# Performance work log

Measured on AMD Instinct MI355X. Metric: run time of the kernel, lower is better.

Reference implementation:

```python
import jax, jax.numpy as jnp
import numpy as np

HEADS = 8
C_HEAD = 64  # head dim == in_dim of x
P0, P1 = 2, 3  # adaptive pool output


def setup_inputs() -> dict:
    key = jax.random.key(0)
    ks = jax.random.split(key, 8)
    b, c, h, w = 16, 64, 64, 96
    m, d = 6, 192
    inner = HEADS * C_HEAD  # 512
    return {
        "x": jax.random.normal(ks[0], (b, c, h, w), dtype=jnp.float32),
        "z": jax.random.normal(ks[1], (b, m, d), dtype=jnp.float32),
        "conv_w": jax.random.normal(ks[2], (192, c), dtype=jnp.float32) * 0.02,
        "conv_b": jax.random.normal(ks[3], (192,), dtype=jnp.float32) * 0.02,
        "wq": jax.random.normal(ks[4], (d, inner), dtype=jnp.float32) * 0.02,
        "bq": jax.random.normal(ks[5], (inner,), dtype=jnp.float32) * 0.02,
        "wo": jax.random.normal(ks[6], (inner, d), dtype=jnp.float32) * 0.02,
        "bo": jax.random.normal(ks[7], (d,), dtype=jnp.float32) * 0.02,
    }


def reference(x, z, conv_w, conv_b, wq, bq, wo, bo):
    b, c, h, w = x.shape
    _, m, d = z.shape
    # 1x1 conv (pointwise GEMM over channels) + bias
    xp = jnp.einsum('bchw,oc->bohw', x, conv_w) + conv_b[None, :, None, None]
    # AdaptiveAvgPool2d((2,3)) with exact divisibility -> block mean
    xp = xp.reshape(b, 192, P0, h // P0, P1, w // P1).mean(axis=(3, 5))  # [b,192,2,3]
    # view(b, d, m) then permute(0,2,1) -> [b, m, d]
    z = z + xp.reshape(b, d, m).transpose(0, 2, 1)
    # k = v: view(b, h*w, c), repeat heads along last dim, view(b, heads, h*w, c)
    # (row-major reshape reproduces torch .view semantics exactly)
    kv = jnp.tile(x.reshape(b, h * w, c), (1, 1, HEADS)).reshape(b, HEADS, h * w, C_HEAD)
    # q = Linear(dim, heads*c) then view(b, heads, m, c)
    q = (z @ wq + bq).reshape(b, HEADS, m, C_HEAD)
    scale = C_HEAD ** -0.5
    dots = jnp.einsum('bhmc,bhlc->bhml', q, kv) * scale  # [b,h,m,l]
    attn = jax.nn.softmax(dots, axis=-1)
    out = jnp.einsum('bhml,bhlc->bhmc', attn, kv)
    out = out.transpose(0, 2, 1, 3).reshape(b, m, HEADS * C_HEAD)  # b m (h c)
    return z + out @ wo + bo
```

## Files before the change

### kernel.cpp

```cpp
#include <hip/hip_runtime.h>

#define NB 16
#define NC 64
#define NM 6
#define ND 192
#define NHEADS 8
#define NCH 64
#define NINNER 512
#define PLANE 6144
#define XB (NC*PLANE)
#define NKEY 768
#define NCHUNK 8
#define CK 96
#define KP 68
#define SP 100

__global__ __launch_bounds__(256) void pool_kernel(const float* __restrict__ x,
                                                   float* __restrict__ xmean) {
    int bc = blockIdx.x;
    const float4* p = (const float4*)(x + (size_t)bc * PLANE);
    int tid = threadIdx.x;
    float acc[6] = {0.f,0.f,0.f,0.f,0.f,0.f};
    #pragma unroll
    for (int k = 0; k < 6; ++k) {
        int idx4 = tid + k * 256;
        int hh = idx4 / 24;
        int w4 = idx4 - hh * 24;
        int j = (hh >> 5) * 3 + (w4 >> 3);
        float4 v = p[idx4];
        acc[j] += v.x + v.y + v.z + v.w;
    }
    int lane = tid & 63, wave = tid >> 6;
    #pragma unroll
    for (int j = 0; j < 6; ++j) {
        float v = acc[j];
        for (int off = 32; off > 0; off >>= 1) v += __shfl_down(v, off, 64);
        acc[j] = v;
    }
    __shared__ float part[4][6];
    if (lane == 0) {
        #pragma unroll
        for (int j = 0; j < 6; ++j) part[wave][j] = acc[j];
    }
    __syncthreads();
    if (tid < 6) {
        float s = part[0][tid] + part[1][tid] + part[2][tid] + part[3][tid];
        xmean[bc * 6 + tid] = s * (1.0f / 1024.0f);
    }
}

__global__ __launch_bounds__(256) void zq_kernel(const float* __restrict__ z,
                                                 const float* __restrict__ conv_w,
                                                 const float* __restrict__ conv_b,
                                                 const float* __restrict__ wq,
                                                 const float* __restrict__ bq,
                                                 const float* __restrict__ xmean,
                                                 float* __restrict__ znew,
                                                 float* __restrict__ qr) {
    int blk = blockIdx.x;
    int cgrp = blk & 7, bm = blk >> 3;
    int b = bm / NM, m = bm - b * NM;
    int tid = threadIdx.x;
    __shared__ float xm[NC];
    __shared__ float zn[ND];
    __shared__ float qpart[3][64];
    if (tid < NC) xm[tid] = xmean[(b * NC + tid) * NM + m];
    __syncthreads();
    if (tid < ND) {
        float a = conv_b[tid];
        const float* wr = conv_w + tid * NC;
        #pragma unroll 16
        for (int c = 0; c < NC; ++c) a += wr[c] * xm[c];
        float v = z[bm * ND + tid] + a;
        zn[tid] = v;
        if (cgrp == 0) znew[bm * ND + tid] = v;
    }
    __syncthreads();
    int colL = tid & 63, ks = tid >> 6;
    int col = cgrp * 64 + colL;
    float a = (ks == 0) ? bq[col] : 0.f;
    int d0 = ks * 48;
    #pragma unroll 8
    for (int d = d0; d < d0 + 48; ++d) a += zn[d] * wq[d * NINNER + col];
    if (ks > 0) qpart[ks - 1][colL] = a;
    __syncthreads();
    if (ks == 0) {
        float tot = a + qpart[0][colL] + qpart[1][colL] + qpart[2][colL];
        int t = m * 8 + cgrp;
        qr[b * (48 * 64) + t * 64 + colL] = tot;
    }
}

__global__ __launch_bounds__(256, 4) void fattn_kernel(const float* __restrict__ x,
                                                       const float* __restrict__ qr,
                                                       float* __restrict__ po,
                                                       float* __restrict__ ps) {
    int blk = blockIdx.x;
    int chunk = blk & 7, bh = blk >> 3;
    int head = bh & 7, b = bh >> 3;
    int tid = threadIdx.x;
    __shared__ float k_lds[CK][KP];
    __shared__ float q_lds[NM][KP];
    __shared__ float s_lds[NM][SP];
    __shared__ float pvp[3][NM][NCH];
    const float* kbase = x + (size_t)b * XB + (size_t)(head * NKEY + chunk * CK) * NCH;

    for (int i = tid; i < NM * NCH; i += 256) {
        int mi = i >> 6, ch = i & 63;
        q_lds[mi][ch] = qr[b * (48 * 64) + (head * NM + mi) * 64 + ch];
    }
    const float4* k4 = (const float4*)kbase;
    #pragma unroll
    for (int r = 0; r < 6; ++r) {
        int i = tid + r * 256;
        int row = i >> 4, c4 = i & 15;
        float4 v = k4[i];
        *(float4*)&k_lds[row][c4 * 4] = v;
    }
    __syncthreads();

    if (tid < 48) {
        int t = tid >> 1, mip = (tid & 1) * 3;
        float a[4][3];
        #pragma unroll
        for (int j = 0; j < 4; ++j) { a[j][0] = 0.f; a[j][1] = 0.f; a[j][2] = 0.f; }
        #pragma unroll 4
        for (int c = 0; c < 16; ++c) {
            float4 q0 = *(const float4*)&q_lds[mip + 0][c * 4];
            float4 q1 = *(const float4*)&q_lds[mip + 1][c * 4];
            float4 q2 = *(const float4*)&q_lds[mip + 2][c * 4];
            #pragma unroll
            for (int j = 0; j < 4; ++j) {
                float4 kv = *(const float4*)&k_lds[t + 24 * j][c * 4];
                a[j][0] += kv.x*q0.x + kv.y*q0.y + kv.z*q0.z + kv.w*q0.w;
                a[j][1] += kv.x*q1.x + kv.y*q1.y + kv.z*q1.z + kv.w*q1.w;
                a[j][2] += kv.x*q2.x + kv.y*q2.y + kv.z*q2.z + kv.w*q2.w;
            }
        }
        #pragma unroll
        for (int j = 0; j < 4; ++j) {
            s_lds[mip + 0][t + 24 * j] = __expf(a[j][0] * 0.125f);
            s_lds[mip + 1][t + 24 * j] = __expf(a[j][1] * 0.125f);
            s_lds[mip + 2][t + 24 * j] = __expf(a[j][2] * 0.125f);
        }
    }
    __syncthreads();

    int lane = tid & 63, wave = tid >> 6;

    #pragma unroll
    for (int rb = 0; rb < 2; ++rb) {
        int mi = rb * 4 + wave;
        if (mi < NM) {
            float v = s_lds[mi][lane] + ((lane < 32) ? s_lds[mi][64 + lane] : 0.f);
            for (int msk = 1; msk < 64; msk <<= 1) v += __shfl_xor(v, msk, 64);
            if (lane == 0) ps[blk * NM + mi] = v;
        }
    }

    float acc[NM] = {0.f,0.f,0.f,0.f,0.f,0.f};
    {
        int uq = tid >> 6, ch = tid & 63;
        int u0 = uq * 24;
        #pragma unroll
        for (int ub = 0; ub < 6; ++ub) {
            float4 s0 = *(const float4*)&s_lds[0][u0 + ub * 4];
            float4 s1 = *(const float4*)&s_lds[1][u0 + ub * 4];
            float4 s2 = *(const float4*)&s_lds[2][u0 + ub * 4];
            float4 s3 = *(const float4*)&s_lds[3][u0 + ub * 4];
            float4 s4 = *(const float4*)&s_lds[4][u0 + ub * 4];
            float4 s5 = *(const float4*)&s_lds[5][u0 + ub * 4];
            float kv0 = k_lds[u0 + ub * 4 + 0][ch];
            float kv1 = k_lds[u0 + ub * 4 + 1][ch];
            float kv2 = k_lds[u0 + ub * 4 + 2][ch];
            float kv3 = k_lds[u0 + ub * 4 + 3][ch];
            acc[0] += s0.x*kv0 + s0.y*kv1 + s0.z*kv2 + s0.w*kv3;
            acc[1] += s1.x*kv0 + s1.y*kv1 + s1.z*kv2 + s1.w*kv3;
            acc[2] += s2.x*kv0 + s2.y*kv1 + s2.z*kv2 + s2.w*kv3;
            acc[3] += s3.x*kv0 + s3.y*kv1 + s3.z*kv2 + s3.w*kv3;
            acc[4] += s4.x*kv0 + s4.y*kv1 + s4.z*kv2 + s4.w*kv3;
            acc[5] += s5.x*kv0 + s5.y*kv1 + s5.z*kv2 + s5.w*kv3;
        }
        if (uq > 0) {
            #pragma unroll
            for (int mo = 0; mo < NM; ++mo) pvp[uq - 1][mo][ch] = acc[mo];
        }
    }
    __syncthreads();
    if (tid < 64) {
        int ch = tid;
        #pragma unroll
        for (int mo = 0; mo < NM; ++mo) {
            float o = acc[mo] + pvp[0][mo][ch] + pvp[1][mo][ch] + pvp[2][mo][ch];
            po[(size_t)blk * (NM * NCH) + mo * NCH + ch] = o;
        }
    }
}

__global__ __launch_bounds__(256) void proj_kernel(const float* __restrict__ znew,
                                                   const float* __restrict__ po,
                                                   const float* __restrict__ ps,
                                                   const float* __restrict__ wo,
                                                   const float* __restrict__ bo,
                                                   float* __restrict__ out) {
    int blk = blockIdx.x;
    int cgrp = blk & 3, bm = blk >> 2;
    int b = bm / NM, m = bm - b * NM;
    int tid = threadIdx.x;
    __shared__ float orow[NINNER];
    __shared__ float part[3][48];

    for (int i = tid; i < NINNER; i += 256) {
        int h = i >> 6, ch = i & 63;
        int base = (b * NHEADS + h) * NCHUNK;
        float num = 0.f, den = 0.f;
        #pragma unroll
        for (int c = 0; c < NCHUNK; ++c) {
            num += po[(size_t)(base + c) * (NM * NCH) + m * NCH + ch];
            den += ps[(base + c) * NM + m];
        }
        orow[i] = num / den;
    }
    __syncthreads();

    int ks = tid / 48;
    int colL = tid - ks * 48;
    float a = 0.f;
    int col = cgrp * 48 + ((tid < 192) ? colL : 0);
    if (tid < 192) {
        int i0 = ks * 128;
        #pragma unroll 8
        for (int i = i0; i < i0 + 128; ++i) a += orow[i] * wo[i * ND + col];
        if (ks > 0) part[ks - 1][colL] = a;
    }
    __syncthreads();
    if (tid < 48) {
        float tot = a + part[0][colL] + part[1][colL] + part[2][colL]
                  + bo[col] + znew[bm * ND + col];
        out[bm * ND + col] = tot;
    }
}

extern "C" void kernel_launch(void* const* d_in, const int* in_sizes, int n_in,
                              void* d_out, int out_size, void* d_ws, size_t ws_size,
                              hipStream_t stream) {
    const float* x      = (const float*)d_in[0];
    const float* z      = (const float*)d_in[1];
    const float* conv_w = (const float*)d_in[2];
    const float* conv_b = (const float*)d_in[3];
    const float* wq     = (const float*)d_in[4];
    const float* bq     = (const float*)d_in[5];
    const float* wo     = (const float*)d_in[6];
    const float* bo     = (const float*)d_in[7];
    float* out = (float*)d_out;

    float* ws    = (float*)d_ws;
    float* xmean = ws;
    float* znew  = ws + 6144;
    float* qr    = ws + 24576;
    float* po    = ws + 73728;
    float* ps    = ws + 466944;

    pool_kernel<<<NB*NC, 256, 0, stream>>>(x, xmean);
    zq_kernel<<<NB*NM*8, 256, 0, stream>>>(z, conv_w, conv_b, wq, bq, xmean, znew, qr);
    fattn_kernel<<<NB*NHEADS*NCHUNK, 256, 0, stream>>>(x, qr, po, ps);
    proj_kernel<<<NB*NM*4, 256, 0, stream>>>(znew, po, ps, wo, bo, out);
}
```

Before: 36.73 us.

## Fuse four stages into one cooperative kernel with grid syncs, keeping x in LDS

Replaces the four separate launches (pool, z/q projection, flash-attention chunks, output projection) with one cooperative kernel of 512 blocks of 512 threads. Stages are separated by grid.sync. Each block stages its x plane into shared memory during pooling and reuses it for attention, so x is not read from global memory twice. This removes launch gaps and one pass over x, at the cost of grid-wide barriers and low occupancy in the light middle and final stages. It falls back to the old four-kernel path if the occupancy check or the cooperative launch fails.

```diff
diff --git a/kernel.cpp b/kernel.cpp
--- a/kernel.cpp
+++ b/kernel.cpp
@@ -1,4 +1,7 @@
 #include <hip/hip_runtime.h>
+#include <hip/hip_cooperative_groups.h>
+
+namespace cg = cooperative_groups;
 
 #define NB 16
 #define NC 64
@@ -14,6 +17,221 @@
 #define CK 96
 #define KP 68
 #define SP 100
+
+#define KP2 72
+#define KSZ (CK*KP2)
+#define QOFF 6912
+#define SOFF 7296
+#define SUBF 7872
+
+__global__ __launch_bounds__(512, 4) void fused_kernel(
+    const float* __restrict__ x, const float* __restrict__ z,
+    const float* __restrict__ conv_w, const float* __restrict__ conv_b,
+    const float* __restrict__ wq, const float* __restrict__ bq,
+    const float* __restrict__ wo, const float* __restrict__ bo,
+    float* __restrict__ xmean, float* __restrict__ znew,
+    float* __restrict__ qr, float* __restrict__ po, float* __restrict__ ps,
+    float* __restrict__ out)
+{
+    cg::grid_group grid = cg::this_grid();
+    int bc = blockIdx.x;
+    int tid = threadIdx.x;
+    int sub = tid >> 8, ttid = tid & 255;
+    int lane = tid & 63;
+    int wsub = (tid >> 6) & 3;
+
+    __shared__ __align__(16) float smem[2 * SUBF];
+    float* S = smem + sub * SUBF;
+
+    int plane = bc + sub * 512;
+    int pb = plane >> 6, pc = plane & 63;
+    int phead = pc >> 3;
+
+    {
+        const float4* p = (const float4*)(x + (size_t)plane * PLANE);
+        float4 v[6];
+        #pragma unroll
+        for (int r = 0; r < 6; ++r) v[r] = p[ttid + r * 256];
+        float acc[6] = {0.f,0.f,0.f,0.f,0.f,0.f};
+        #pragma unroll
+        for (int r = 0; r < 6; ++r) {
+            int idx4 = ttid + r * 256;
+            int hh = idx4 / 24;
+            int w4 = idx4 - hh * 24;
+            int j = (hh >> 5) * 3 + (w4 >> 3);
+            acc[j] += v[r].x + v[r].y + v[r].z + v[r].w;
+            int u = idx4 >> 4, c4 = idx4 & 15;
+            *(float4*)&S[u * KP2 + c4 * 4] = v[r];
+        }
+        #pragma unroll
+        for (int j = 0; j < 6; ++j) {
+            float s = acc[j];
+            for (int off = 32; off > 0; off >>= 1) s += __shfl_down(s, off, 64);
+            acc[j] = s;
+        }
+        if (lane == 0) {
+            #pragma unroll
+            for (int j = 0; j < 6; ++j) S[QOFF + wsub * 6 + j] = acc[j];
+        }
+        __syncthreads();
+        if (ttid < 6) {
+            float s = S[QOFF + ttid] + S[QOFF + 6 + ttid]
+                    + S[QOFF + 12 + ttid] + S[QOFF + 18 + ttid];
+            xmean[plane * 6 + ttid] = s * (1.0f / 1024.0f);
+        }
+    }
+    __threadfence();
+    grid.sync();
+    __threadfence();
+
+    {
+        int task = bc + sub * 512;
+        bool act = task < 768;
+        int cgrp = task & 7, bm = task >> 3;
+        int b = bm / NM, m = bm - b * NM;
+        float* xm = S + QOFF;
+        float* zn = S + QOFF + 64;
+        float* qp = S + QOFF + 256;
+        if (act && ttid < NC) xm[ttid] = xmean[(b * NC + ttid) * NM + m];
+        __syncthreads();
+        if (act && ttid < ND) {
+            float a = conv_b[ttid];
+            const float* wr = conv_w + ttid * NC;
+            #pragma unroll 16
+            for (int cc = 0; cc < NC; ++cc) a += wr[cc] * xm[cc];
+            float vv = z[bm * ND + ttid] + a;
+            zn[ttid] = vv;
+            if (cgrp == 0) znew[bm * ND + ttid] = vv;
+        }
+        __syncthreads();
+        int colL = ttid & 63, ks = ttid >> 6;
+        int col = cgrp * 64 + colL;
+        float a = 0.f;
+        if (act) {
+            a = (ks == 0) ? bq[col] : 0.f;
+            int d0 = ks * 48;
+            #pragma unroll 8
+            for (int d = d0; d < d0 + 48; ++d) a += zn[d] * wq[d * NINNER + col];
+            if (ks > 0) qp[(ks - 1) * 64 + colL] = a;
+        }
+        __syncthreads();
+        if (act && ks == 0) {
+            float tot = a + qp[colL] + qp[64 + colL] + qp[128 + colL];
+            int t = m * 8 + cgrp;
+            qr[b * (48 * 64) + t * 64 + colL] = tot;
+        }
+    }
+    __threadfence();
+    grid.sync();
+    __threadfence();
+
+    {
+        for (int i = ttid; i < NM * NCH; i += 256) {
+            int mi = i >> 6, ch = i & 63;
+            S[QOFF + mi * 64 + ch] = qr[pb * (48 * 64) + (phead * NM + mi) * 64 + ch];
+        }
+        __syncthreads();
+
+        if (ttid < 48) {
+            int t = ttid >> 1, mip = (ttid & 1) * 3;
+            float a[4][3];
+            #pragma unroll
+            for (int j = 0; j < 4; ++j) { a[j][0]=0.f; a[j][1]=0.f; a[j][2]=0.f; }
+            #pragma unroll 4
+            for (int cc = 0; cc < 16; ++cc) {
+                float4 q0 = *(const float4*)&S[QOFF + (mip + 0) * 64 + cc * 4];
+                float4 q1 = *(const float4*)&S[QOFF + (mip + 1) * 64 + cc * 4];
+                float4 q2 = *(const float4*)&S[QOFF + (mip + 2) * 64 + cc * 4];
+                #pragma unroll
+                for (int j = 0; j < 4; ++j) {
+                    float4 kv = *(const float4*)&S[(t + 24 * j) * KP2 + cc * 4];
+                    a[j][0] += kv.x*q0.x + kv.y*q0.y + kv.z*q0.z + kv.w*q0.w;
+                    a[j][1] += kv.x*q1.x + kv.y*q1.y + kv.z*q1.z + kv.w*q1.w;
+                    a[j][2] += kv.x*q2.x + kv.y*q2.y + kv.z*q2.z + kv.w*q2.w;
+                }
+            }
+            #pragma unroll
+            for (int j = 0; j < 4; ++j) {
+                S[SOFF + (mip + 0) * 96 + t + 24 * j] = __expf(a[j][0] * 0.125f);
+                S[SOFF + (mip + 1) * 96 + t + 24 * j] = __expf(a[j][1] * 0.125f);
+                S[SOFF + (mip + 2) * 96 + t + 24 * j] = __expf(a[j][2] * 0.125f);
+            }
+        }
+        __syncthreads();
+
+        #pragma unroll
+        for (int rb = 0; rb < 2; ++rb) {
+            int mi = rb * 4 + wsub;
+            if (mi < NM) {
+                float v = S[SOFF + mi * 96 + lane]
+                        + ((lane < 32) ? S[SOFF + mi * 96 + 64 + lane] : 0.f);
+                for (int msk = 1; msk < 64; msk <<= 1) v += __shfl_xor(v, msk, 64);
+                if (lane == 0) ps[plane * NM + mi] = v;
+            }
+        }
+
+        {
+            int chL = lane & 15, rg = lane >> 4;
+            int ch = wsub * 16 + chL;
+            float acc[NM] = {0.f,0.f,0.f,0.f,0.f,0.f};
+            #pragma unroll 8
+            for (int j = 0; j < 24; ++j) {
+                int u = rg + 4 * j;
+                float kv = S[u * KP2 + ch];
+                #pragma unroll
+                for (int mo = 0; mo < NM; ++mo) acc[mo] += S[SOFF + mo * 96 + u] * kv;
+            }
+            #pragma unroll
+            for (int mo = 0; mo < NM; ++mo) {
+                float v = acc[mo];
+                v += __shfl_xor(v, 16, 64);
+                v += __shfl_xor(v, 32, 64);
+                if (rg == 0) po[(size_t)plane * (NM * NCH) + mo * NCH + ch] = v;
+            }
+        }
+    }
+    __threadfence();
+    grid.sync();
+    __threadfence();
+
+    {
+        bool act = (sub == 0) && (bc < 384);
+        int cgrp = bc & 3, bm = bc >> 2;
+        int b = bm / NM, m = bm - b * NM;
+        float* orow = S + QOFF;
+        float* part = S + QOFF + 512;
+        if (act) {
+            for (int i = ttid; i < NINNER; i += 256) {
+                int h = i >> 6, ch = i & 63;
+                int base = (b * NHEADS + h) * NCHUNK;
+                float num = 0.f, den = 0.f;
+                #pragma unroll
+                for (int cu = 0; cu < NCHUNK; ++cu) {
+                    num += po[(size_t)(base + cu) * (NM * NCH) + m * NCH + ch];
+                    den += ps[(base + cu) * NM + m];
+                }
+                orow[i] = num / den;
+            }
+        }
+        __syncthreads();
+        int ks = ttid / 48;
+        int colL = ttid - ks * 48;
+        float a = 0.f;
+        int col = cgrp * 48 + ((ttid < 192) ? colL : 0);
+        if (act && ttid < 192) {
+            int i0 = ks * 128;
+            #pragma unroll 8
+            for (int i = i0; i < i0 + 128; ++i) a += orow[i] * wo[i * ND + col];
+            if (ks > 0) part[(ks - 1) * 48 + colL] = a;
+        }
+        __syncthreads();
+        if (act && ttid < 48) {
+            float tot = a + part[colL] + part[48 + colL] + part[96 + colL]
+                      + bo[col] + znew[bm * ND + col];
+            out[bm * ND + col] = tot;
+        }
+    }
+}
 
 __global__ __launch_bounds__(256) void pool_kernel(const float* __restrict__ x,
                                                    float* __restrict__ xmean) {
@@ -147,7 +365,6 @@
     __syncthreads();
 
     int lane = tid & 63, wave = tid >> 6;
-
     #pragma unroll
     for (int rb = 0; rb < 2; ++rb) {
         int mi = rb * 4 + wave;
@@ -261,6 +478,27 @@
     float* po    = ws + 73728;
     float* ps    = ws + 466944;
 
+    static int coop_state = -1;
+    if (coop_state == -1) {
+        int nb = 0;
+        hipError_t e = hipOccupancyMaxActiveBlocksPerMultiprocessor(
+            &nb, (const void*)fused_kernel, 512, 0);
+        coop_state = (e == hipSuccess && nb >= 2) ? 1 : 0;
+    }
+    if (coop_state == 1) {
+        void* args[] = {
+            (void*)&x, (void*)&z, (void*)&conv_w, (void*)&conv_b,
+            (void*)&wq, (void*)&bq, (void*)&wo, (void*)&bo,
+            (void*)&xmean, (void*)&znew, (void*)&qr, (void*)&po, (void*)&ps,
+            (void*)&out
+        };
+        hipError_t e = hipLaunchCooperativeKernel((const void*)fused_kernel,
+                                                  dim3(512), dim3(512),
+                                                  args, 0, stream);
+        if (e == hipSuccess) return;
+        coop_state = 0;
+    }
+
     pool_kernel<<<NB*NC, 256, 0, stream>>>(x, xmean);
     zq_kernel<<<NB*NM*8, 256, 0, stream>>>(z, conv_w, conv_b, wq, bq, xmean, znew, qr);
     fattn_kernel<<<NB*NHEADS*NCHUNK, 256, 0, stream>>>(x, qr, po, ps);
```

After: 36.66 us. About the same (-0.2%).

## Process all six query rows per block in zq_kernel to reuse wq loads

Applied to the files above, without the earlier changes.

zq_kernel now handles all NM=6 query rows of a batch in one block instead of one block per (b,m), so the grid drops from 768 to 128 blocks. Each wq element loaded from global memory is reused across six accumulators, cutting wq traffic by a factor of six. The cost is fewer blocks (less parallelism on a large GPU) and redundant conv recomputation, since every cgrp block still computes the full 6x192 conv for its batch.

```diff
diff --git a/kernel.cpp b/kernel.cpp
--- a/kernel.cpp
+++ b/kernel.cpp
@@ -58,36 +58,51 @@
                                                  float* __restrict__ znew,
                                                  float* __restrict__ qr) {
     int blk = blockIdx.x;
-    int cgrp = blk & 7, bm = blk >> 3;
-    int b = bm / NM, m = bm - b * NM;
-    int tid = threadIdx.x;
-    __shared__ float xm[NC];
-    __shared__ float zn[ND];
-    __shared__ float qpart[3][64];
-    if (tid < NC) xm[tid] = xmean[(b * NC + tid) * NM + m];
-    __syncthreads();
-    if (tid < ND) {
-        float a = conv_b[tid];
-        const float* wr = conv_w + tid * NC;
+    int b = blk >> 3, cgrp = blk & 7;
+    int tid = threadIdx.x;
+    __shared__ float xm_s[NC * NM];
+    __shared__ float zn_s[NM * ND];
+    __shared__ float qpart[3][NM][64];
+
+    for (int i = tid; i < NC * NM; i += 256) xm_s[i] = xmean[b * (NC * NM) + i];
+    __syncthreads();
+
+    for (int i = tid; i < NM * ND; i += 256) {
+        int m = i / ND, d = i - m * ND;
+        float a = conv_b[d];
+        const float* wr = conv_w + d * NC;
         #pragma unroll 16
-        for (int c = 0; c < NC; ++c) a += wr[c] * xm[c];
-        float v = z[bm * ND + tid] + a;
-        zn[tid] = v;
-        if (cgrp == 0) znew[bm * ND + tid] = v;
-    }
-    __syncthreads();
+        for (int c = 0; c < NC; ++c) a += wr[c] * xm_s[c * NM + m];
+        float v = z[(b * NM + m) * ND + d] + a;
+        zn_s[i] = v;
+        if (cgrp == 0) znew[b * (NM * ND) + i] = v;
+    }
+    __syncthreads();
+
     int colL = tid & 63, ks = tid >> 6;
     int col = cgrp * 64 + colL;
-    float a = (ks == 0) ? bq[col] : 0.f;
+    float acc[NM] = {0.f,0.f,0.f,0.f,0.f,0.f};
     int d0 = ks * 48;
-    #pragma unroll 8
-    for (int d = d0; d < d0 + 48; ++d) a += zn[d] * wq[d * NINNER + col];
-    if (ks > 0) qpart[ks - 1][colL] = a;
+    #pragma unroll 4
+    for (int d = d0; d < d0 + 48; ++d) {
+        float wv = wq[d * NINNER + col];
+        #pragma unroll
+        for (int m = 0; m < NM; ++m) acc[m] += zn_s[m * ND + d] * wv;
+    }
+    if (ks > 0) {
+        #pragma unroll
+        for (int m = 0; m < NM; ++m) qpart[ks - 1][m][colL] = acc[m];
+    }
     __syncthreads();
     if (ks == 0) {
-        float tot = a + qpart[0][colL] + qpart[1][colL] + qpart[2][colL];
-        int t = m * 8 + cgrp;
-        qr[b * (48 * 64) + t * 64 + colL] = tot;
+        float bias = bq[col];
+        #pragma unroll
+        for (int m = 0; m < NM; ++m) {
+            float tot = acc[m] + qpart[0][m][colL] + qpart[1][m][colL]
+                      + qpart[2][m][colL] + bias;
+            int t = m * 8 + cgrp;
+            qr[b * (48 * 64) + t * 64 + colL] = tot;
+        }
     }
 }
 
@@ -147,7 +162,6 @@
     __syncthreads();
 
     int lane = tid & 63, wave = tid >> 6;
-
     #pragma unroll
     for (int rb = 0; rb < 2; ++rb) {
         int mi = rb * 4 + wave;
@@ -262,7 +276,7 @@
     float* ps    = ws + 466944;
 
     pool_kernel<<<NB*NC, 256, 0, stream>>>(x, xmean);
-    zq_kernel<<<NB*NM*8, 256, 0, stream>>>(z, conv_w, conv_b, wq, bq, xmean, znew, qr);
+    zq_kernel<<<NB*8, 256, 0, stream>>>(z, conv_w, conv_b, wq, bq, xmean, znew, qr);
     fattn_kernel<<<NB*NHEADS*NCHUNK, 256, 0, stream>>>(x, qr, po, ps);
     proj_kernel<<<NB*NM*4, 256, 0, stream>>>(znew, po, ps, wo, bo, out);
 }
```

New measurement: 42.80 us. 1.17x slower.
